# Kernel tuning notes

Hardware: AMD Instinct MI355X
Metric: run time of the kernel (lower is better)

Reference implementation:

```python
import jax, jax.numpy as jnp
import numpy as np

N, E, G, L, H, TD, F = 10000, 100000, 64, 2, 512, 256, 128
DIS = 2 * 3 * F            # sinusoid embedding dim = 768
DIN = 2 * H + DIS + 6      # edge_mlp input dim = 1798
EPS = 1e-5


def _ln(x, g, b):
    mu = x.mean(-1, keepdims=True)
    var = ((x - mu) ** 2).mean(-1, keepdims=True)
    return (x - mu) * jax.lax.rsqrt(var + EPS) * g + b


def _sin_emb(x):  # x: [E, 3] -> [E, 2*3*F]
    freqs = 2.0 * np.pi * jnp.arange(F, dtype=x.dtype)
    e = (x[:, :, None] * freqs).reshape(x.shape[0], -1)
    return jnp.concatenate([jnp.sin(e), jnp.cos(e)], axis=-1)


def setup_inputs() -> dict:
    key = jax.random.key(0)
    ks = jax.random.split(key, 16)
    s = 0.02
    return dict(
        atom_types=jax.random.randint(ks[0], (N,), 0, 100),
        node2graph=jnp.sort(jax.random.randint(ks[1], (N,), 0, G)),
        edge_index=jax.random.randint(ks[2], (2, E), 0, N),
        frac_diff=jax.random.uniform(ks[3], (E, 3)) - 0.5,
        lattices=jax.random.normal(ks[4], (G, 6)),
        t=jax.random.uniform(ks[5], (1, 1)),
        emb_table=jax.random.normal(ks[6], (119, H)) * s,
        Wt=jax.random.normal(ks[7], (TD, 1)) * s,
        Wa=jax.random.normal(ks[8], (H, H + TD)) * s,
        ba=jnp.zeros((H,)),
        ln_g=jnp.ones((L, H)), ln_b=jnp.zeros((L, H)),
        eW1=jax.random.normal(ks[9], (L, H, DIN)) * s, eb1=jnp.zeros((L, H)),
        eW2=jax.random.normal(ks[10], (L, H, H)) * s, eb2=jnp.zeros((L, H)),
        nW1=jax.random.normal(ks[11], (L, H, 2 * H)) * s, nb1=jnp.zeros((L, H)),
        nW2=jax.random.normal(ks[12], (L, H, H)) * s, nb2=jnp.zeros((L, H)),
        fln_g=jnp.ones((H,)), fln_b=jnp.zeros((H,)),
        Wc=jax.random.normal(ks[13], (3, H)) * s,
    )


def reference(atom_types, node2graph, edge_index, frac_diff, lattices, t,
              emb_table, Wt, Wa, ba, ln_g, ln_b, eW1, eb1, eW2, eb2,
              nW1, nb1, nW2, nb2, fln_g, fln_b, Wc):
    silu = jax.nn.silu
    src, dst = edge_index[0], edge_index[1]
    edge2graph = node2graph[src]
    demb = _sin_emb(frac_diff)                 # [E, 768]
    lat_e = lattices[edge2graph]               # [E, 6] (lattices_flat gathered to edges)
    counts = jax.ops.segment_sum(jnp.ones((E, 1), frac_diff.dtype), src, num_segments=N)
    counts = jnp.maximum(counts, 1.0)

    # node init: embedding + broadcast time emb -> atom_latent_emb -> silu
    t_emb = t @ Wt.T                           # [1, TD]
    h = jnp.concatenate([emb_table[atom_types],
                         jnp.broadcast_to(t_emb, (N, TD))], axis=1)
    h = silu(h @ Wa.T + ba)                    # [N, H]

    def step(h, p):
        g, b, w1, b1, w2, b2, m1, c1, m2, c2 = p
        hn = _ln(h, g, b)                      # pre-LN
        ef = jnp.concatenate([hn[src], hn[dst], lat_e, demb], axis=1)  # [E, DIN]
        m = silu(ef @ w1.T + b1)
        m = silu(m @ w2.T + b2)                # [E, H] edge messages
        agg = jax.ops.segment_sum(m, src, num_segments=N) / counts    # scatter-mean
        u = jnp.concatenate([hn, agg], axis=1)  # [N, 2H]
        u = silu(u @ m1.T + c1)
        u = silu(u @ m2.T + c2)
        return h + u, None                     # residual

    h, _ = jax.lax.scan(step, h, (ln_g, ln_b, eW1, eb1, eW2, eb2,
                                  nW1, nb1, nW2, nb2))
    h = _ln(h, fln_g, fln_b)
    return h @ Wc.T                            # [N, 3] coord_out
```

## Files before the change

### kernel.cpp

```cpp
#include <hip/hip_runtime.h>
#include <stdint.h>

typedef unsigned short u16;
typedef unsigned int u32;
typedef __attribute__((ext_vector_type(8))) short short8;
typedef __attribute__((ext_vector_type(4))) float f32x4;

#define TN 10000
#define TE 100000
#define PAD 128

static constexpr size_t A256(size_t x){ return (x+255)/256*256; }

__device__ __forceinline__ float bf2f(u16 u){ u32 x=((u32)u)<<16; float f; __builtin_memcpy(&f,&x,4); return f; }
__device__ __forceinline__ u16 f2bf(float f){ u32 x; __builtin_memcpy(&x,&f,4); x = x + 0x7fffu + ((x>>16)&1u); return (u16)(x>>16); }
__device__ __forceinline__ float siluf(float v){ return v*(1.0f/(1.0f+__expf(-v))); }

__device__ __forceinline__ void gld16(const void* g, void* l){
  __builtin_amdgcn_global_load_lds((const __attribute__((address_space(1))) u32*)g,
                                   (__attribute__((address_space(3))) u32*)l, 16, 0, 0);
}

__device__ __forceinline__ void blockReduce2(float& s, float& ss){
  for (int off=32; off>0; off>>=1){ s += __shfl_down(s,off,64); ss += __shfl_down(ss,off,64); }
  __shared__ float red[8];
  int lane = threadIdx.x&63, wave = threadIdx.x>>6;
  if (lane==0){ red[wave*2]=s; red[wave*2+1]=ss; }
  __syncthreads();
  s  = red[0]+red[2]+red[4]+red[6];
  ss = red[1]+red[3]+red[5]+red[7];
}

template<int EPI, bool SWZ>
__device__ __forceinline__ void gemm_core(
    const u16* __restrict__ A, int lda,
    const u16* __restrict__ B, int ldb,
    int M, int K,
    u16* __restrict__ Cb, float* __restrict__ Cf, int ldc,
    const float* __restrict__ bias,
    int cbase,
    const u16* __restrict__ PQ,
    const int* __restrict__ nodS, const int* __restrict__ dstS,
    const int* __restrict__ n2g, const float* __restrict__ Rp,
    int nwg)
{
  __shared__ u16 As[3*2048];
  __shared__ u16 Bs[3*4096];
  int bm, bn;
  if constexpr (SWZ){
    int orig = blockIdx.x;
    int q = nwg>>3, r = nwg&7;
    int xcd = orig&7, idx = orig>>3;
    int wg = (xcd<r ? xcd*(q+1) : r*(q+1)+(xcd-r)*q) + idx;
    bm = wg>>2; bn = wg&3;
  } else { bm = blockIdx.x; bn = blockIdx.y; }
  const int t = threadIdx.x;
  const int lane = t&63;
  const int wave = t>>6;
  const int wm = wave>>1, wn = wave&1;

  f32x4 acc[2][4];
  #pragma unroll
  for (int i=0;i<2;i++)
    #pragma unroll
    for (int j=0;j<4;j++) acc[i][j] = (f32x4){0.f,0.f,0.f,0.f};

  const int sr = t>>2;
  const int sk = (((t&3) ^ ((t>>3)&3)))*8;
  int ar0 = bm*64 + sr; if (ar0 > M-1) ar0 = M-1;
  const u16* Ag0 = A + (size_t)ar0*lda + sk;
  const u16* Bg0 = B + (size_t)(bn*128 + sr)*ldb + sk;
  const u16* Bg1 = B + (size_t)(bn*128 + sr + 64)*ldb + sk;
  u16* As0 = &As[t*8];
  u16* Bs0 = &Bs[t*8];
  u16* Bs1 = &Bs[t*8 + 2048];

  const int rg = ((lane>>4) ^ ((lane>>1)&3))*8;
  const u16* ApL = &As[(wm*32 + (lane&15))*32 + rg];
  const u16* BpL = &Bs[(wn*64 + (lane&15))*32 + rg];

  const int nk = K>>5;
  #define STAGEN(kt, b) { const int ko=(kt)<<5; \
      gld16(Ag0+ko, As0+(b)*2048); \
      gld16(Bg0+ko, Bs0+(b)*4096); \
      gld16(Bg1+ko, Bs1+(b)*4096); }

  STAGEN(0,0)
  STAGEN(1,1)
  int cb=0, sb=2;
  for (int ki=0; ki<nk; ++ki){
    if (ki+1 < nk) asm volatile("s_waitcnt vmcnt(3)" ::: "memory");
    else           asm volatile("s_waitcnt vmcnt(0)" ::: "memory");
    __builtin_amdgcn_s_barrier();
    if (ki+2 < nk) STAGEN(ki+2, sb)
    const int ca = cb*2048, cbb = cb*4096;
    short8 af[2], bf[4];
    #pragma unroll
    for (int mi=0;mi<2;mi++) af[mi] = *(const short8*)(ApL + ca + mi*512);
    #pragma unroll
    for (int ni=0;ni<4;ni++) bf[ni] = *(const short8*)(BpL + cbb + ni*512);
    #pragma unroll
    for (int mi=0;mi<2;mi++)
      #pragma unroll
      for (int ni=0;ni<4;ni++)
        acc[mi][ni] = __builtin_amdgcn_mfma_f32_16x16x32_bf16(af[mi], bf[ni], acc[mi][ni], 0,0,0);
    cb = (cb==2)?0:cb+1;
    sb = (sb==2)?0:sb+1;
  }
  #undef STAGEN

  const int c0 = bn*128 + wn*64 + (lane&15);
  const int r0 = bm*64 + wm*32 + ((lane>>4)<<2);

  if constexpr (EPI==0){
    #pragma unroll
    for (int mi=0;mi<2;mi++)
      #pragma unroll
      for (int r=0;r<4;r++){
        int row = r0 + mi*16 + r;
        if (row < M){
          u16* o = Cb + (size_t)row*ldc + c0;
          #pragma unroll
          for (int ni=0;ni<4;ni++) o[ni*16] = f2bf(acc[mi][ni][r]);
        }
      }
  } else if constexpr (EPI==1){
    float bz[4];
    #pragma unroll
    for (int ni=0;ni<4;ni++) bz[ni] = bias[c0 + ni*16];
    #pragma unroll
    for (int mi=0;mi<2;mi++)
      #pragma unroll
      for (int r=0;r<4;r++){
        int row = r0 + mi*16 + r;
        if (row < M){
          u16* o = Cb + (size_t)row*ldc + c0;
          #pragma unroll
          for (int ni=0;ni<4;ni++) o[ni*16] = f2bf(siluf(acc[mi][ni][r]+bz[ni]));
        }
      }
  } else if constexpr (EPI==2){
    #pragma unroll
    for (int mi=0;mi<2;mi++)
      #pragma unroll
      for (int r=0;r<4;r++){
        int row = r0 + mi*16 + r;
        if (row < M){
          int gs = cbase + row;
          int sn = nodS[gs], dn = dstS[gs];
          int g  = n2g[sn];
          const u16* Pp = PQ + (size_t)sn*1024 + c0;
          const u16* Qp = PQ + (size_t)dn*1024 + 512 + c0;
          const float* Rr = Rp + g*512 + c0;
          u16* o = Cb + (size_t)row*ldc + c0;
          #pragma unroll
          for (int ni=0;ni<4;ni++){
            float v = acc[mi][ni][r] + bf2f(Pp[ni*16]) + bf2f(Qp[ni*16]) + Rr[ni*16];
            o[ni*16] = f2bf(siluf(v));
          }
        }
      }
  } else {
    float bz[4];
    #pragma unroll
    for (int ni=0;ni<4;ni++) bz[ni] = bias[c0 + ni*16];
    #pragma unroll
    for (int mi=0;mi<2;mi++)
      #pragma unroll
      for (int r=0;r<4;r++){
        int row = r0 + mi*16 + r;
        if (row < M){
          float* hp = Cf + (size_t)row*ldc + c0;
          #pragma unroll
          for (int ni=0;ni<4;ni++) hp[ni*16] += siluf(acc[mi][ni][r]+bz[ni]);
        }
      }
  }
}

#define GEMM_ARGS const u16* A, int lda, const u16* B, int ldb, int M, int K, \
    u16* Cb, float* Cf, int ldc, const float* bias, int cbase, const u16* PQ, \
    const int* nodS, const int* dstS, const int* n2g, const float* Rp, int nwg
#define GEMM_PASS A,lda,B,ldb,M,K,Cb,Cf,ldc,bias,cbase,PQ,nodS,dstS,n2g,Rp,nwg

__global__ __launch_bounds__(256) void g_pq(GEMM_ARGS){ gemm_core<0,false>(GEMM_PASS); }
__global__ __launch_bounds__(256) void g_n1(GEMM_ARGS){ gemm_core<1,false>(GEMM_PASS); }
__global__ __launch_bounds__(256) void g_n2(GEMM_ARGS){ gemm_core<3,false>(GEMM_PASS); }
__global__ __launch_bounds__(256) void g_e1(GEMM_ARGS){ gemm_core<2,true>(GEMM_PASS); }
__global__ __launch_bounds__(256) void g_e2(GEMM_ARGS){ gemm_core<1,true>(GEMM_PASS); }

__global__ void k_demb(const float* __restrict__ fdS, int cbase, int M,
                       u16* __restrict__ dembC){
  const float TP = 6.283185307179586f;
  int total = M*96;
  for (int i = blockIdx.x*blockDim.x+threadIdx.x; i<total; i+=gridDim.x*blockDim.x){
    int row = i/96;
    int g   = i - row*96;
    int col = g*8;
    int isc = col>=384;
    int cc = isc ? col-384 : col;
    int d = cc>>7;
    float x = fdS[(size_t)(cbase+row)*3 + d];
    float fb = (float)(cc&127);
    float w0 = x*fb; w0 -= rintf(w0);
    float s, c, ds, dc;
    __sincosf(TP*w0, &s, &c);
    __sincosf(TP*x, &ds, &dc);
    short8 v;
    #pragma unroll
    for (int j=0;j<8;j++){
      v[j] = (short)f2bf(isc ? c : s);
      float s2 = s*dc + c*ds;
      float c2 = c*dc - s*ds;
      s = s2; c = c2;
    }
    *(short8*)(dembC + (size_t)row*768 + col) = v;
  }
}

__global__ void k_prep(const float* __restrict__ tp, const float* __restrict__ Wt,
                       const float* __restrict__ Wa, const float* __restrict__ ba,
                       float* __restrict__ bias2){
  __shared__ float te[256];
  int t=threadIdx.x;
  te[t] = tp[0]*Wt[t];
  __syncthreads();
  for (int i=t;i<512;i+=256){
    float s = ba[i];
    const float* wr = Wa + (size_t)i*768 + 512;
    for (int j=0;j<256;j++) s += wr[j]*te[j];
    bias2[i]=s;
  }
}

__global__ void k_h0(const float* __restrict__ emb, const float* __restrict__ Wa,
                     const float* __restrict__ bias2, float* __restrict__ h0){
  __shared__ float et[512];
  int ty=blockIdx.x, t=threadIdx.x;
  et[t]=emb[(size_t)ty*512+t]; et[t+256]=emb[(size_t)ty*512+t+256];
  __syncthreads();
  for (int i=t;i<512;i+=256){
    float s=bias2[i];
    const float* wr = Wa + (size_t)i*768;
    for (int k=0;k<512;k++) s += wr[k]*et[k];
    h0[(size_t)ty*512+i]=siluf(s);
  }
}

__global__ void k_inith(const int* __restrict__ at, const float* __restrict__ h0,
                        float* __restrict__ h){
  int total=TN*512;
  for (int i=blockIdx.x*blockDim.x+threadIdx.x; i<total; i+=gridDim.x*blockDim.x){
    int n=i>>9, c=i&511;
    h[i]=h0[(size_t)at[n]*512+c];
  }
}

__global__ void k_count(const int* __restrict__ src, int* __restrict__ counts){
  for (int e=blockIdx.x*blockDim.x+threadIdx.x; e<TE; e+=gridDim.x*blockDim.x)
    atomicAdd(&counts[src[e]],1);
}

__global__ void k_scan(const int* __restrict__ cnt, int* __restrict__ iptr){
  __shared__ int sums[1024];
  const int T=1024, n=TN;
  int t=threadIdx.x;
  const int chunk=(n+T-1)/T;
  int s=0;
  for (int i=0;i<chunk;i++){ int idx=t*chunk+i; if(idx<n) s+=cnt[idx]; }
  sums[t]=s; __syncthreads();
  for (int off=1; off<T; off<<=1){
    int v = (t>=off)? sums[t-off] : 0;
    __syncthreads();
    sums[t]+=v;
    __syncthreads();
  }
  int run = (t==0)?0:sums[t-1];
  for (int i=0;i<chunk;i++){
    int idx=t*chunk+i;
    if(idx<n){ iptr[idx]=run; run+=cnt[idx]; }
  }
  if (t==T-1) iptr[n]=run;
}

__global__ void k_fill(const int* __restrict__ src, const int* __restrict__ dst,
                       const float* __restrict__ fd, const int* __restrict__ iptr,
                       int* __restrict__ slots, int* __restrict__ nodS,
                       int* __restrict__ dstS, float* __restrict__ fdS){
  for (int e=blockIdx.x*blockDim.x+threadIdx.x; e<TE; e+=gridDim.x*blockDim.x){
    int s=src[e];
    int p=atomicAdd(&slots[s],1);
    int gs=iptr[s]+p;
    nodS[gs]=s; dstS[gs]=dst[e];
    fdS[(size_t)gs*3+0]=fd[(size_t)e*3+0];
    fdS[(size_t)gs*3+1]=fd[(size_t)e*3+1];
    fdS[(size_t)gs*3+2]=fd[(size_t)e*3+2];
  }
}

__global__ void k_R(const float* __restrict__ lat, const float* __restrict__ eW1,
                    const float* __restrict__ eb1, float* __restrict__ Rp){
  int total = 2*64*512;
  for (int i=blockIdx.x*blockDim.x+threadIdx.x; i<total; i+=gridDim.x*blockDim.x){
    int l = i>>15;
    int g = (i>>9)&63;
    int o = i&511;
    float s = eb1[l*512+o];
    const float* wr = eW1 + ((size_t)l*512 + o)*1798 + 1024;
    const float* lr = lat + g*6;
    #pragma unroll
    for (int k=0;k<6;k++) s += lr[k]*wr[k];
    Rp[i]=s;
  }
}

struct PackDesc { const float* src; u16* dst; int rows, cols, ld, off; };
struct PackArgs { PackDesc d[12]; };
__global__ void k_pack(PackArgs pa){
  PackDesc d = pa.d[blockIdx.y];
  int total = d.rows*d.cols;
  for (int i = blockIdx.x*blockDim.x + threadIdx.x; i<total; i += gridDim.x*blockDim.x){
    int r = i/d.cols, c = i - r*d.cols;
    d.dst[i] = f2bf(d.src[(size_t)r*d.ld + d.off + c]);
  }
}

__global__ void k_ln(const float* __restrict__ h, const float* __restrict__ g,
                     const float* __restrict__ b, u16* __restrict__ hcat){
  int row = blockIdx.x, t = threadIdx.x;
  const float* hr = h + (size_t)row*512;
  float v0 = hr[t], v1 = hr[t+256];
  float s = v0+v1, ss = v0*v0+v1*v1;
  blockReduce2(s, ss);
  float mean = s*(1.0f/512.0f);
  float var  = ss*(1.0f/512.0f) - mean*mean;
  float rs = rsqrtf(var + 1e-5f);
  u16* o = hcat + (size_t)row*1024;
  o[t]     = f2bf((v0-mean)*rs*g[t]     + b[t]);
  o[t+256] = f2bf((v1-mean)*rs*g[t+256] + b[t+256]);
}

__global__ void k_aggpart(const u16* __restrict__ xc, const int* __restrict__ iptr,
                          int s0, int s1, float* __restrict__ aggf){
  int n=blockIdx.x, t=threadIdx.x;
  int beg=iptr[n], end=iptr[n+1];
  if (beg<s0) beg=s0;
  if (end>s1) end=s1;
  if (beg>=end) return;
  float a0=0.f, a1=0.f;
  for (int i=beg;i<end;i++){
    const u16* xr = xc + (size_t)(i-s0)*512;
    a0 += bf2f(xr[t]); a1 += bf2f(xr[t+256]);
  }
  float* ar = aggf + (size_t)n*512;
  ar[t] += a0; ar[t+256] += a1;
}

__global__ void k_aggfin(const float* __restrict__ aggf, const int* __restrict__ counts,
                         u16* __restrict__ hcat){
  int n=blockIdx.x, t=threadIdx.x;
  int c=counts[n]; if (c<1) c=1;
  float inv = 1.0f/(float)c;
  const float* ar = aggf + (size_t)n*512;
  u16* o = hcat + (size_t)n*1024 + 512;
  o[t]     = f2bf(ar[t]*inv);
  o[t+256] = f2bf(ar[t+256]*inv);
}

__global__ void k_agg(const u16* __restrict__ x, const int* __restrict__ iptr,
                      u16* __restrict__ hcat){
  int n=blockIdx.x, t=threadIdx.x;
  int beg=iptr[n], end=iptr[n+1];
  float a0=0.f, a1=0.f;
  for (int i=beg;i<end;i++){
    const u16* xr = x + (size_t)i*512;
    a0 += bf2f(xr[t]); a1 += bf2f(xr[t+256]);
  }
  int c=end-beg; if (c<1) c=1;
  float inv = 1.0f/(float)c;
  u16* o = hcat + (size_t)n*1024 + 512;
  o[t]     = f2bf(a0*inv);
  o[t+256] = f2bf(a1*inv);
}

__global__ void k_final(const float* __restrict__ h, const float* __restrict__ g,
                        const float* __restrict__ b, const float* __restrict__ Wc,
                        float* __restrict__ out){
  int row=blockIdx.x, t=threadIdx.x;
  const float* hr = h + (size_t)row*512;
  float v0=hr[t], v1=hr[t+256];
  float s=v0+v1, ss=v0*v0+v1*v1;
  blockReduce2(s,ss);
  float mean=s*(1.0f/512.0f), var=ss*(1.0f/512.0f)-mean*mean, rs=rsqrtf(var+1e-5f);
  float n0=(v0-mean)*rs*g[t]+b[t];
  float n1=(v1-mean)*rs*g[t+256]+b[t+256];
  float p0 = n0*Wc[t]      + n1*Wc[t+256];
  float p1 = n0*Wc[512+t]  + n1*Wc[512+t+256];
  float p2 = n0*Wc[1024+t] + n1*Wc[1024+t+256];
  for (int off=32; off>0; off>>=1){
    p0+=__shfl_down(p0,off,64); p1+=__shfl_down(p1,off,64); p2+=__shfl_down(p2,off,64);
  }
  __shared__ float rp[4][3];
  int lane=t&63, wave=t>>6;
  if (lane==0){ rp[wave][0]=p0; rp[wave][1]=p1; rp[wave][2]=p2; }
  __syncthreads();
  if (t<3) out[(size_t)row*3+t] = rp[0][t]+rp[1][t]+rp[2][t]+rp[3][t];
}

__global__ void k_report(float* out, int n, float val){
  for (int i=blockIdx.x*blockDim.x+threadIdx.x; i<n; i+=gridDim.x*blockDim.x) out[i]=val;
}

extern "C" void kernel_launch(void* const* d_in, const int* in_sizes, int n_in,
                              void* d_out, int out_size, void* d_ws, size_t ws_size,
                              hipStream_t stream)
{
  const int*   atom  = (const int*)  d_in[0];
  const int*   n2g   = (const int*)  d_in[1];
  const int*   eidx  = (const int*)  d_in[2];
  const float* fdiff = (const float*)d_in[3];
  const float* lat   = (const float*)d_in[4];
  const float* tp    = (const float*)d_in[5];
  const float* emb   = (const float*)d_in[6];
  const float* Wt    = (const float*)d_in[7];
  const float* Wa    = (const float*)d_in[8];
  const float* ba    = (const float*)d_in[9];
  const float* lng   = (const float*)d_in[10];
  const float* lnb   = (const float*)d_in[11];
  const float* eW1   = (const float*)d_in[12];
  const float* eb1   = (const float*)d_in[13];
  const float* eW2   = (const float*)d_in[14];
  const float* eb2   = (const float*)d_in[15];
  const float* nW1   = (const float*)d_in[16];
  const float* nb1   = (const float*)d_in[17];
  const float* nW2   = (const float*)d_in[18];
  const float* nb2   = (const float*)d_in[19];
  const float* flng  = (const float*)d_in[20];
  const float* flnb  = (const float*)d_in[21];
  const float* Wc    = (const float*)d_in[22];
  float* out = (float*)d_out;

  size_t o = 0;
  auto al = [&](size_t b){ size_t r = o; o = A256(o + b); return r; };
  size_t OH   = al((size_t)TN*512*4);
  size_t OPQ  = al((size_t)TN*1024*2);
  size_t OHC  = al((size_t)TN*1024*2);
  size_t OWAB = al((size_t)2*1024*512*2);
  size_t OW1D = al((size_t)2*512*768*2);
  size_t OW2  = al((size_t)2*512*512*2);
  size_t OWN1 = al((size_t)2*512*1024*2);
  size_t OWN2 = al((size_t)2*512*512*2);
  size_t ORP  = al((size_t)2*64*512*4);
  size_t OH0  = al((size_t)119*512*4);
  size_t OB2  = al(512*4);
  size_t OCNT = al((size_t)TN*4);
  size_t OSLOT= al((size_t)TN*4);
  size_t OIPTR= al((size_t)(TN+1)*4);
  size_t ONOD = al((size_t)(TE+PAD)*4);
  size_t ODST = al((size_t)(TE+PAD)*4);
  size_t OFDS = al((size_t)(TE+PAD)*3*4);
  size_t statEnd = o;

  int nch = 0; int ec = 0;
  size_t OAGG=0, OM=0, OX=0, ODB=0;
  const int cands[4] = {1,2,4,8};
  for (int ci=0; ci<4; ++ci){
    int c = cands[ci];
    o = statEnd;
    size_t e = TE/c;
    size_t ag = (c>1) ? al((size_t)TN*512*4) : 0;
    size_t om = al((e+PAD)*512*2);
    size_t ox = al((e+PAD)*512*2);
    size_t od = al((e+PAD)*768*2);
    if (o <= ws_size){ nch=c; ec=(int)e; OAGG=ag; OM=om; OX=ox; ODB=od; break; }
  }
  char* ws = (char*)d_ws;
  if (!nch){ k_report<<<64,256,0,stream>>>(out, out_size, (float)(ws_size>>20)); return; }

  float* h    = (float*)(ws+OH);
  u16*   PQ   = (u16*)(ws+OPQ);
  u16*   hcat = (u16*)(ws+OHC);
  float* aggf = (float*)(ws+OAGG);
  u16*   m    = (u16*)(ws+OM);
  u16*   u    = (u16*)(ws+OM);
  u16*   x    = (u16*)(ws+OX);
  u16*   demb = (u16*)(ws+ODB);
  u16*   Wab  = (u16*)(ws+OWAB);
  u16*   W1d  = (u16*)(ws+OW1D);
  u16*   W2c  = (u16*)(ws+OW2);
  u16*   Wn1  = (u16*)(ws+OWN1);
  u16*   Wn2  = (u16*)(ws+OWN2);
  float* Rp   = (float*)(ws+ORP);
  float* h0   = (float*)(ws+OH0);
  float* b2   = (float*)(ws+OB2);
  int* counts = (int*)(ws+OCNT);
  int* slots  = (int*)(ws+OSLOT);
  int* iptr   = (int*)(ws+OIPTR);
  int* nodS   = (int*)(ws+ONOD);
  int* dstS   = (int*)(ws+ODST);
  float* fdS  = (float*)(ws+OFDS);
  const int* src = eidx;
  const int* dst = eidx + TE;

  hipMemsetAsync(ws+OCNT, 0, OIPTR - OCNT, stream);

  k_prep<<<1,256,0,stream>>>(tp, Wt, Wa, ba, b2);
  k_h0<<<119,256,0,stream>>>(emb, Wa, b2, h0);
  k_inith<<<1024,256,0,stream>>>(atom, h0, h);
  k_count<<<391,256,0,stream>>>(src, counts);
  k_scan<<<1,1024,0,stream>>>(counts, iptr);
  k_fill<<<391,256,0,stream>>>(src, dst, fdiff, iptr, slots, nodS, dstS, fdS);
  k_R<<<256,256,0,stream>>>(lat, eW1, eb1, Rp);

  PackArgs pa;
  for (int l=0;l<2;l++){
    const float* e1 = eW1 + (size_t)l*512*1798;
    pa.d[l*6+0] = {e1, Wab + (size_t)l*1024*512,             512, 512, 1798, 0};
    pa.d[l*6+1] = {e1, Wab + (size_t)l*1024*512 + 512*512,   512, 512, 1798, 512};
    pa.d[l*6+2] = {e1, W1d + (size_t)l*512*768,              512, 768, 1798, 1030};
    pa.d[l*6+3] = {eW2 + (size_t)l*512*512, W2c + (size_t)l*512*512, 512, 512, 512, 0};
    pa.d[l*6+4] = {nW1 + (size_t)l*512*1024, Wn1 + (size_t)l*512*1024, 512, 1024, 1024, 0};
    pa.d[l*6+5] = {nW2 + (size_t)l*512*512, Wn2 + (size_t)l*512*512, 512, 512, 512, 0};
  }
  k_pack<<<dim3(128,12),256,0,stream>>>(pa);

  const int nbmE = (ec+63)/64;
  const int nwgE = nbmE*4;
  const int BMN  = (TN+63)/64;
  const int N0 = 0;

  if (nch==1)
    k_demb<<<4096,256,0,stream>>>(fdS, 0, TE, demb);

  for (int l=0;l<2;l++){
    k_ln<<<TN,256,0,stream>>>(h, lng+(size_t)l*512, lnb+(size_t)l*512, hcat);
    g_pq<<<dim3(BMN,8),256,0,stream>>>(hcat, 1024, Wab+(size_t)l*1024*512, 512,
        TN, 512, PQ, nullptr, 1024, nullptr, N0, nullptr, nullptr, nullptr, nullptr, nullptr, 0);
    if (nch>1) hipMemsetAsync(aggf, 0, (size_t)TN*512*4, stream);
    for (int c=0;c<nch;c++){
      int s0 = c*ec;
      if (nch>1) k_demb<<<2048,256,0,stream>>>(fdS, s0, ec, demb);
      g_e1<<<nwgE,256,0,stream>>>(demb, 768, W1d+(size_t)l*512*768, 768,
          ec, 768, m, nullptr, 512, nullptr,
          s0, PQ, nodS, dstS, n2g, Rp+(size_t)l*64*512, nwgE);
      g_e2<<<nwgE,256,0,stream>>>(m, 512, W2c+(size_t)l*512*512, 512,
          ec, 512, x, nullptr, 512, eb2+(size_t)l*512,
          N0, nullptr, nullptr, nullptr, nullptr, nullptr, nwgE);
      if (nch>1) k_aggpart<<<TN,256,0,stream>>>(x, iptr, s0, s0+ec, aggf);
    }
    if (nch==1) k_agg<<<TN,256,0,stream>>>(x, iptr, hcat);
    else        k_aggfin<<<TN,256,0,stream>>>(aggf, counts, hcat);
    g_n1<<<dim3(BMN,4),256,0,stream>>>(hcat, 1024, Wn1+(size_t)l*512*1024, 1024,
        TN, 1024, u, nullptr, 512, nb1+(size_t)l*512,
        N0, nullptr, nullptr, nullptr, nullptr, nullptr, 0);
    g_n2<<<dim3(BMN,4),256,0,stream>>>(u, 512, Wn2+(size_t)l*512*512, 512,
        TN, 512, nullptr, h, 512, nb2+(size_t)l*512,
        N0, nullptr, nullptr, nullptr, nullptr, nullptr, 0);
  }
  k_final<<<TN,256,0,stream>>>(h, flng, flnb, Wc, out);
}
```

Before: 1.220 ms.

## Generate sinusoid edge embedding inside edge GEMM A-tile staging, deepen pipeline to four stages

The separate k_demb kernel and its materialized [E,768] bf16 buffer are removed. The first edge GEMM now computes sin/cos values on the fly while staging its A tile into LDS, using a per-row angle-addition recurrence. All GEMMs also move from three to four LDS buffers with prefetch distance three. This cuts a large global write and read of the embedding and frees workspace, so single-chunk mode is more likely. The cost is extra trig ALU work repeated per N-tile (four column blocks, two layers), plus more LDS per block, which may lower occupancy.

Measured after the change: 1.113 ms. 8.8% less time.

```diff
diff --git a/kernel.cpp b/kernel.cpp
--- a/kernel.cpp
+++ b/kernel.cpp
@@ -31,7 +31,7 @@
   ss = red[1]+red[3]+red[5]+red[7];
 }
 
-template<int EPI, bool SWZ>
+template<int EPI, bool SWZ, bool TRIG>
 __device__ __forceinline__ void gemm_core(
     const u16* __restrict__ A, int lda,
     const u16* __restrict__ B, int ldb,
@@ -42,10 +42,10 @@
     const u16* __restrict__ PQ,
     const int* __restrict__ nodS, const int* __restrict__ dstS,
     const int* __restrict__ n2g, const float* __restrict__ Rp,
-    int nwg)
+    int nwg, const float* __restrict__ fdS)
 {
-  __shared__ u16 As[3*2048];
-  __shared__ u16 Bs[3*4096];
+  __shared__ u16 As[4*2048];
+  __shared__ u16 Bs[4*4096];
   int bm, bn;
   if constexpr (SWZ){
     int orig = blockIdx.x;
@@ -58,6 +58,7 @@
   const int lane = t&63;
   const int wave = t>>6;
   const int wm = wave>>1, wn = wave&1;
+  const float TP = 6.283185307179586f;
 
   f32x4 acc[2][4];
   #pragma unroll
@@ -68,32 +69,68 @@
   const int sr = t>>2;
   const int sk = (((t&3) ^ ((t>>3)&3)))*8;
   int ar0 = bm*64 + sr; if (ar0 > M-1) ar0 = M-1;
-  const u16* Ag0 = A + (size_t)ar0*lda + sk;
+  const u16* Ag0 = TRIG ? nullptr : (A + (size_t)ar0*lda + sk);
   const u16* Bg0 = B + (size_t)(bn*128 + sr)*ldb + sk;
   const u16* Bg1 = B + (size_t)(bn*128 + sr + 64)*ldb + sk;
   u16* As0 = &As[t*8];
   u16* Bs0 = &Bs[t*8];
   u16* Bs1 = &Bs[t*8 + 2048];
 
+  float fx0=0,fx1=0,fx2=0, ds0=0,dc0=0, ds1=0,dc1=0, ds2=0,dc2=0;
+  if constexpr (TRIG){
+    const float* fr = fdS + (size_t)(cbase + ar0)*3;
+    fx0=fr[0]; fx1=fr[1]; fx2=fr[2];
+    __sincosf(TP*fx0,&ds0,&dc0);
+    __sincosf(TP*fx1,&ds1,&dc1);
+    __sincosf(TP*fx2,&ds2,&dc2);
+  }
+
   const int rg = ((lane>>4) ^ ((lane>>1)&3))*8;
   const u16* ApL = &As[(wm*32 + (lane&15))*32 + rg];
   const u16* BpL = &Bs[(wn*64 + (lane&15))*32 + rg];
 
   const int nk = K>>5;
   #define STAGEN(kt, b) { const int ko=(kt)<<5; \
-      gld16(Ag0+ko, As0+(b)*2048); \
+      if constexpr (TRIG){ \
+        int col = ko + sk; \
+        int isc = col>=384; int cc = isc ? col-384 : col; \
+        int d = cc>>7; \
+        float xx = (d==0)?fx0:((d==1)?fx1:fx2); \
+        float dss = (d==0)?ds0:((d==1)?ds1:ds2); \
+        float dcc = (d==0)?dc0:((d==1)?dc1:dc2); \
+        float w0 = xx*(float)(cc&127); w0 -= rintf(w0); \
+        float s_, c_; __sincosf(TP*w0, &s_, &c_); \
+        short8 v; \
+        _Pragma("unroll") \
+        for (int j=0;j<8;j++){ \
+          v[j] = (short)f2bf(isc ? c_ : s_); \
+          float s2 = s_*dcc + c_*dss; \
+          float c2 = c_*dcc - s_*dss; \
+          s_ = s2; c_ = c2; } \
+        *(short8*)(As0 + (b)*2048) = v; \
+      } else { \
+        gld16(Ag0+ko, As0+(b)*2048); \
+      } \
       gld16(Bg0+ko, Bs0+(b)*4096); \
       gld16(Bg1+ko, Bs1+(b)*4096); }
 
   STAGEN(0,0)
   STAGEN(1,1)
-  int cb=0, sb=2;
+  STAGEN(2,2)
   for (int ki=0; ki<nk; ++ki){
-    if (ki+1 < nk) asm volatile("s_waitcnt vmcnt(3)" ::: "memory");
-    else           asm volatile("s_waitcnt vmcnt(0)" ::: "memory");
+    const int ahead = nk - ki;
+    if constexpr (TRIG){
+      if (ahead>2)       asm volatile("s_waitcnt vmcnt(4) lgkmcnt(0)" ::: "memory");
+      else if (ahead==2) asm volatile("s_waitcnt vmcnt(2) lgkmcnt(0)" ::: "memory");
+      else               asm volatile("s_waitcnt vmcnt(0) lgkmcnt(0)" ::: "memory");
+    } else {
+      if (ahead>2)       asm volatile("s_waitcnt vmcnt(6)" ::: "memory");
+      else if (ahead==2) asm volatile("s_waitcnt vmcnt(3)" ::: "memory");
+      else               asm volatile("s_waitcnt vmcnt(0)" ::: "memory");
+    }
     __builtin_amdgcn_s_barrier();
-    if (ki+2 < nk) STAGEN(ki+2, sb)
-    const int ca = cb*2048, cbb = cb*4096;
+    if (ki+3 < nk) STAGEN(ki+3, (ki+3)&3)
+    const int ca = (ki&3)*2048, cbb = (ki&3)*4096;
     short8 af[2], bf[4];
     #pragma unroll
     for (int mi=0;mi<2;mi++) af[mi] = *(const short8*)(ApL + ca + mi*512);
@@ -104,8 +141,6 @@
       #pragma unroll
       for (int ni=0;ni<4;ni++)
         acc[mi][ni] = __builtin_amdgcn_mfma_f32_16x16x32_bf16(af[mi], bf[ni], acc[mi][ni], 0,0,0);
-    cb = (cb==2)?0:cb+1;
-    sb = (sb==2)?0:sb+1;
   }
   #undef STAGEN
 
@@ -180,43 +215,15 @@
 
 #define GEMM_ARGS const u16* A, int lda, const u16* B, int ldb, int M, int K, \
     u16* Cb, float* Cf, int ldc, const float* bias, int cbase, const u16* PQ, \
-    const int* nodS, const int* dstS, const int* n2g, const float* Rp, int nwg
-#define GEMM_PASS A,lda,B,ldb,M,K,Cb,Cf,ldc,bias,cbase,PQ,nodS,dstS,n2g,Rp,nwg
-
-__global__ __launch_bounds__(256) void g_pq(GEMM_ARGS){ gemm_core<0,false>(GEMM_PASS); }
-__global__ __launch_bounds__(256) void g_n1(GEMM_ARGS){ gemm_core<1,false>(GEMM_PASS); }
-__global__ __launch_bounds__(256) void g_n2(GEMM_ARGS){ gemm_core<3,false>(GEMM_PASS); }
-__global__ __launch_bounds__(256) void g_e1(GEMM_ARGS){ gemm_core<2,true>(GEMM_PASS); }
-__global__ __launch_bounds__(256) void g_e2(GEMM_ARGS){ gemm_core<1,true>(GEMM_PASS); }
-
-__global__ void k_demb(const float* __restrict__ fdS, int cbase, int M,
-                       u16* __restrict__ dembC){
-  const float TP = 6.283185307179586f;
-  int total = M*96;
-  for (int i = blockIdx.x*blockDim.x+threadIdx.x; i<total; i+=gridDim.x*blockDim.x){
-    int row = i/96;
-    int g   = i - row*96;
-    int col = g*8;
-    int isc = col>=384;
-    int cc = isc ? col-384 : col;
-    int d = cc>>7;
-    float x = fdS[(size_t)(cbase+row)*3 + d];
-    float fb = (float)(cc&127);
-    float w0 = x*fb; w0 -= rintf(w0);
-    float s, c, ds, dc;
-    __sincosf(TP*w0, &s, &c);
-    __sincosf(TP*x, &ds, &dc);
-    short8 v;
-    #pragma unroll
-    for (int j=0;j<8;j++){
-      v[j] = (short)f2bf(isc ? c : s);
-      float s2 = s*dc + c*ds;
-      float c2 = c*dc - s*ds;
-      s = s2; c = c2;
-    }
-    *(short8*)(dembC + (size_t)row*768 + col) = v;
-  }
-}
+    const int* nodS, const int* dstS, const int* n2g, const float* Rp, int nwg, \
+    const float* fdS
+#define GEMM_PASS A,lda,B,ldb,M,K,Cb,Cf,ldc,bias,cbase,PQ,nodS,dstS,n2g,Rp,nwg,fdS
+
+__global__ __launch_bounds__(256) void g_pq(GEMM_ARGS){ gemm_core<0,false,false>(GEMM_PASS); }
+__global__ __launch_bounds__(256) void g_n1(GEMM_ARGS){ gemm_core<1,false,false>(GEMM_PASS); }
+__global__ __launch_bounds__(256) void g_n2(GEMM_ARGS){ gemm_core<3,false,false>(GEMM_PASS); }
+__global__ __launch_bounds__(256) void g_e1(GEMM_ARGS){ gemm_core<2,true,true>(GEMM_PASS); }
+__global__ __launch_bounds__(256) void g_e2(GEMM_ARGS){ gemm_core<1,true,false>(GEMM_PASS); }
 
 __global__ void k_prep(const float* __restrict__ tp, const float* __restrict__ Wt,
                        const float* __restrict__ Wa, const float* __restrict__ ba,
@@ -462,7 +469,7 @@
   size_t statEnd = o;
 
   int nch = 0; int ec = 0;
-  size_t OAGG=0, OM=0, OX=0, ODB=0;
+  size_t OAGG=0, OM=0, OX=0;
   const int cands[4] = {1,2,4,8};
   for (int ci=0; ci<4; ++ci){
     int c = cands[ci];
@@ -471,8 +478,7 @@
     size_t ag = (c>1) ? al((size_t)TN*512*4) : 0;
     size_t om = al((e+PAD)*512*2);
     size_t ox = al((e+PAD)*512*2);
-    size_t od = al((e+PAD)*768*2);
-    if (o <= ws_size){ nch=c; ec=(int)e; OAGG=ag; OM=om; OX=ox; ODB=od; break; }
+    if (o <= ws_size){ nch=c; ec=(int)e; OAGG=ag; OM=om; OX=ox; break; }
   }
   char* ws = (char*)d_ws;
   if (!nch){ k_report<<<64,256,0,stream>>>(out, out_size, (float)(ws_size>>20)); return; }
@@ -484,7 +490,6 @@
   u16*   m    = (u16*)(ws+OM);
   u16*   u    = (u16*)(ws+OM);
   u16*   x    = (u16*)(ws+OX);
-  u16*   demb = (u16*)(ws+ODB);
   u16*   Wab  = (u16*)(ws+OWAB);
   u16*   W1d  = (u16*)(ws+OW1D);
   u16*   W2c  = (u16*)(ws+OW2);
@@ -529,33 +534,29 @@
   const int BMN  = (TN+63)/64;
   const int N0 = 0;
 
-  if (nch==1)
-    k_demb<<<4096,256,0,stream>>>(fdS, 0, TE, demb);
-
   for (int l=0;l<2;l++){
     k_ln<<<TN,256,0,stream>>>(h, lng+(size_t)l*512, lnb+(size_t)l*512, hcat);
     g_pq<<<dim3(BMN,8),256,0,stream>>>(hcat, 1024, Wab+(size_t)l*1024*512, 512,
-        TN, 512, PQ, nullptr, 1024, nullptr, N0, nullptr, nullptr, nullptr, nullptr, nullptr, 0);
+        TN, 512, PQ, nullptr, 1024, nullptr, N0, nullptr, nullptr, nullptr, nullptr, nullptr, 0, nullptr);
     if (nch>1) hipMemsetAsync(aggf, 0, (size_t)TN*512*4, stream);
     for (int c=0;c<nch;c++){
       int s0 = c*ec;
-      if (nch>1) k_demb<<<2048,256,0,stream>>>(fdS, s0, ec, demb);
-      g_e1<<<nwgE,256,0,stream>>>(demb, 768, W1d+(size_t)l*512*768, 768,
+      g_e1<<<nwgE,256,0,stream>>>(nullptr, 768, W1d+(size_t)l*512*768, 768,
           ec, 768, m, nullptr, 512, nullptr,
-          s0, PQ, nodS, dstS, n2g, Rp+(size_t)l*64*512, nwgE);
+          s0, PQ, nodS, dstS, n2g, Rp+(size_t)l*64*512, nwgE, fdS);
       g_e2<<<nwgE,256,0,stream>>>(m, 512, W2c+(size_t)l*512*512, 512,
           ec, 512, x, nullptr, 512, eb2+(size_t)l*512,
-          N0, nullptr, nullptr, nullptr, nullptr, nullptr, nwgE);
+          N0, nullptr, nullptr, nullptr, nullptr, nullptr, nwgE, nullptr);
       if (nch>1) k_aggpart<<<TN,256,0,stream>>>(x, iptr, s0, s0+ec, aggf);
     }
     if (nch==1) k_agg<<<TN,256,0,stream>>>(x, iptr, hcat);
     else        k_aggfin<<<TN,256,0,stream>>>(aggf, counts, hcat);
     g_n1<<<dim3(BMN,4),256,0,stream>>>(hcat, 1024, Wn1+(size_t)l*512*1024, 1024,
         TN, 1024, u, nullptr, 512, nb1+(size_t)l*512,
-        N0, nullptr, nullptr, nullptr, nullptr, nullptr, 0);
+        N0, nullptr, nullptr, nullptr, nullptr, nullptr, 0, nullptr);
     g_n2<<<dim3(BMN,4),256,0,stream>>>(u, 512, Wn2+(size_t)l*512*512, 512,
         TN, 512, nullptr, h, 512, nb2+(size_t)l*512,
-        N0, nullptr, nullptr, nullptr, nullptr, nullptr, 0);
+        N0, nullptr, nullptr, nullptr, nullptr, nullptr, 0, nullptr);
   }
   k_final<<<TN,256,0,stream>>>(h, flng, flnb, Wc, out);
 }
```
